# Optimization experiments

Measured on AMD Instinct MI355X. Metric: run time of the kernel, lower is better.

## Reference

```python
import jax, jax.numpy as jnp
import numpy as np

WIN = 11
K1 = 0.01
K2 = 0.03


def setup_inputs() -> dict:
    key = jax.random.key(0)
    k1, k2 = jax.random.split(key)
    B, C, H, W = 64, 1, 512, 512
    img = jax.random.uniform(k1, (B, C, H, W), dtype=jnp.float32)
    ref = jax.random.uniform(k2, (B, C, H, W), dtype=jnp.float32)
    data_range = jnp.ones((B,), dtype=jnp.float32)
    return {"img": img, "ref": ref, "data_range": data_range}


def _box_filter(x, win):
    w = jnp.ones((1, 1, win, win), dtype=x.dtype) / (win * win)
    pad = win // 2
    return jax.lax.conv_general_dilated(
        x, w, window_strides=(1, 1),
        padding=[(pad, pad), (pad, pad)],
        dimension_numbers=("NCHW", "OIHW", "NCHW"))


def reference(img, ref, data_range):
    dr = data_range[:, None, None, None]
    C1 = (K1 * dr) ** 2
    C2 = (K2 * dr) ** 2
    n_pix = WIN * WIN
    cov_norm = n_pix / (n_pix - 1)

    ux = _box_filter(img, WIN)
    uy = _box_filter(ref, WIN)
    uxx = _box_filter(img * img, WIN)
    uyy = _box_filter(ref * ref, WIN)
    uxy = _box_filter(img * ref, WIN)

    vx = cov_norm * (uxx - ux * ux)
    vy = cov_norm * (uyy - uy * uy)
    vxy = cov_norm * (uxy - ux * uy)

    A1 = 2 * ux * uy + C1
    A2 = 2 * vxy + C2
    B1 = ux ** 2 + uy ** 2 + C1
    B2 = vx + vy + C2
    S = A1 * A2 / (B1 * B2)
    return S
```

## Files before the change

kernel.cpp:

```cpp
#include <hip/hip_runtime.h>


static constexpr int HI = 512, WI = 512;
static constexpr int RS = 16;
static constexpr int SPB = HI / RS;

struct R8 { float4 a, b; };

__device__ __forceinline__ R8 ld8(const float* p) {
  R8 r; r.a = ((const float4*)p)[0]; r.b = ((const float4*)p)[1]; return r;
}

__device__ __forceinline__ void unp(const R8& v, float o[8]) {
  o[0]=v.a.x; o[1]=v.a.y; o[2]=v.a.z; o[3]=v.a.w;
  o[4]=v.b.x; o[5]=v.b.y; o[6]=v.b.z; o[7]=v.b.w;
}

__device__ __forceinline__ float shr1(float x) {
  return __int_as_float(__builtin_amdgcn_update_dpp(
      0, __float_as_int(x), 0x138, 0xf, 0xf, true));
}
__device__ __forceinline__ float shl1(float x) {
  return __int_as_float(__builtin_amdgcn_update_dpp(
      0, __float_as_int(x), 0x130, 0xf, 0xf, true));
}

__device__ __forceinline__ void horiz11(const float v[8], float H[8]) {
  float L[5], R[5];
#pragma unroll
  for (int k = 0; k < 5; ++k) {
    L[k] = shr1(v[3 + k]);
    R[k] = shl1(v[k]);
  }
  float h = (((L[0] + L[1]) + (L[2] + L[3])) + ((L[4] + v[0]) + (v[1] + v[2])))
            + ((v[3] + v[4]) + v[5]);
  H[0] = h;
  h = h - L[0] + v[6]; H[1] = h;
  h = h - L[1] + v[7]; H[2] = h;
  h = h - L[2] + R[0]; H[3] = h;
  h = h - L[3] + R[1]; H[4] = h;
  h = h - L[4] + R[2]; H[5] = h;
  h = h - v[0] + R[3]; H[6] = h;
  h = h - v[1] + R[4]; H[7] = h;
}

__global__ __launch_bounds__(256, 2)
void ssim_wave(const float* __restrict__ img, const float* __restrict__ ref,
               const float* __restrict__ drng, const float* __restrict__ zrow,
               float* __restrict__ out)
{
  int bid = (int)blockIdx.x;
  const int nb = (int)gridDim.x;
  if ((nb & 7) == 0) {
    const int cpx = nb >> 3;
    bid = (bid & 7) * cpx + (bid >> 3);
  }

  const int lane = threadIdx.x & 63;
  const int wv   = bid * 4 + (threadIdx.x >> 6);
  const int b    = wv / SPB;
  const int r0   = (wv % SPB) * RS;
  const int c0   = lane * 8;

  const float dr  = drng[b];
  const float C1  = (0.01f * dr) * (0.01f * dr);
  const float C2  = (0.03f * dr) * (0.03f * dr);
  const float inv_n    = 1.0f / 121.0f;
  const float cov_norm = 121.0f / 120.0f;

  const size_t base = (size_t)b * ((size_t)HI * WI);
  const float* xb = img + base;
  const float* yb = ref + base;
  float*       ob = out + base;

  auto nrow = [&](const float* tb, int t) -> const float* {
    const int r = r0 - 5 + t;
    return (((unsigned)r < (unsigned)HI) ? tb + (size_t)r * WI : zrow) + c0;
  };
  auto orow = [&](const float* tb, int t) -> const float* {
    const int r = r0 - 16 + t;
    return (((unsigned)r < (unsigned)HI) ? tb + (size_t)r * WI : zrow) + c0;
  };

  float Sx[8], Sy[8], Sxx[8], Syy[8], Sxy[8];
#pragma unroll
  for (int c = 0; c < 8; ++c) { Sx[c]=0.f; Sy[c]=0.f; Sxx[c]=0.f; Syy[c]=0.f; Sxy[c]=0.f; }

  auto accA = [&](const float xn[8], const float yn[8]) {
#pragma unroll
    for (int c = 0; c < 8; ++c) {
      Sx[c] += xn[c];  Sy[c] += yn[c];
      Sxx[c] = fmaf(xn[c], xn[c], Sxx[c]);
      Syy[c] = fmaf(yn[c], yn[c], Syy[c]);
      Sxy[c] = fmaf(xn[c], yn[c], Sxy[c]);
    }
  };
  auto accB = [&](const float xn[8], const float yn[8],
                  const float xo[8], const float yo[8]) {
#pragma unroll
    for (int c = 0; c < 8; ++c) {
      Sx[c] += xn[c] - xo[c];
      Sy[c] += yn[c] - yo[c];
      Sxx[c] = fmaf(xn[c], xn[c], fmaf(-xo[c], xo[c], Sxx[c]));
      Syy[c] = fmaf(yn[c], yn[c], fmaf(-yo[c], yo[c], Syy[c]));
      Sxy[c] = fmaf(xn[c], yn[c], fmaf(-xo[c], yo[c], Sxy[c]));
    }
  };

  auto emit = [&](int t) {
    float H0[8], H1[8], H2[8], H3[8], H4[8];
    horiz11(Sx,  H0);
    horiz11(Sy,  H1);
    horiz11(Sxx, H2);
    horiz11(Syy, H3);
    horiz11(Sxy, H4);
    float res[8];
#pragma unroll
    for (int c = 0; c < 8; ++c) {
      const float ux  = H0[c] * inv_n, uy  = H1[c] * inv_n;
      const float uxx = H2[c] * inv_n, uyy = H3[c] * inv_n, uxy = H4[c] * inv_n;
      const float vx  = cov_norm * (uxx - ux * ux);
      const float vy  = cov_norm * (uyy - uy * uy);
      const float vxy = cov_norm * (uxy - ux * uy);
      const float A1 = 2.f * ux * uy + C1;
      const float A2 = 2.f * vxy + C2;
      const float B1 = ux * ux + uy * uy + C1;
      const float B2 = vx + vy + C2;
      res[c] = (A1 * A2) * __builtin_amdgcn_rcpf(B1 * B2);
    }
    const int ro = r0 + t - 10;
    float4* po = (float4*)(ob + (size_t)ro * WI + c0);
    po[0] = make_float4(res[0], res[1], res[2], res[3]);
    po[1] = make_float4(res[4], res[5], res[6], res[7]);
  };

  R8 nx[2], ny[2], ox[2], oy[2];
  nx[0] = ld8(nrow(xb, 0)); ny[0] = ld8(nrow(yb, 0));
  nx[1] = ld8(nrow(xb, 1)); ny[1] = ld8(nrow(yb, 1));

#pragma unroll 2
  for (int t = 0; t < 9; ++t) {
    const int s = t & 1;
    float xn[8], yn[8];
    unp(nx[s], xn); unp(ny[s], yn);
    nx[s] = ld8(nrow(xb, t + 2)); ny[s] = ld8(nrow(yb, t + 2));
    accA(xn, yn);
  }
  {
    float xn[8], yn[8];
    unp(nx[1], xn); unp(ny[1], yn);
    nx[1] = ld8(nrow(xb, 11)); ny[1] = ld8(nrow(yb, 11));
    ox[1] = ld8(orow(xb, 11)); oy[1] = ld8(orow(yb, 11));
    accA(xn, yn);
  }
  {
    float xn[8], yn[8];
    unp(nx[0], xn); unp(ny[0], yn);
    nx[0] = ld8(nrow(xb, 12)); ny[0] = ld8(nrow(yb, 12));
    ox[0] = ld8(orow(xb, 12)); oy[0] = ld8(orow(yb, 12));
    accA(xn, yn);
    emit(10);
  }

  auto stepB = [&](int t, int s, bool issue) {
    float xn[8], yn[8], xo[8], yo[8];
    unp(nx[s], xn); unp(ny[s], yn); unp(ox[s], xo); unp(oy[s], yo);
    if (issue) {
      nx[s] = ld8(nrow(xb, t + 2)); ny[s] = ld8(nrow(yb, t + 2));
      ox[s] = ld8(orow(xb, t + 2)); oy[s] = ld8(orow(yb, t + 2));
    }
    accB(xn, yn, xo, yo);
    emit(t);
  };

#pragma unroll 1
  for (int u = 0; u < 6; ++u) {
    stepB(11 + 2 * u, 1, true);
    stepB(12 + 2 * u, 0, true);
  }
  stepB(23, 1, true);
  stepB(24, 0, false);
  stepB(25, 1, false);
}

extern "C" void kernel_launch(void* const* d_in, const int* in_sizes, int n_in,
                              void* d_out, int out_size, void* d_ws, size_t ws_size,
                              hipStream_t stream)
{
  const float* img = (const float*)d_in[0];
  const float* ref = (const float*)d_in[1];
  const float* drg = (const float*)d_in[2];
  float* out = (float*)d_out;

  (void)hipMemsetAsync(d_ws, 0, (size_t)WI * sizeof(float) + 64, stream);

  const int B = in_sizes[0] / (HI * WI);
  const int waves = B * SPB;
  dim3 grid(waves / 4);
  dim3 block(256);
  hipLaunchKernelGGL(ssim_wave, grid, block, 0, stream,
                     img, ref, drg, (const float*)d_ws, out);
}
```

Baseline: 208.1 us.

## Cache sliding-window rows in an LDS ring instead of reloading from global

Each wave now keeps the last 11 input rows of img and ref in a per-wave LDS ring buffer. The rows leaving the vertical window are read from that ring rather than reloaded from global memory, which removes the second global load stream. In exchange, each block needs about 90 KB of dynamic LDS and the block shrinks to 128 threads, so only about one block (two waves) fits per CU. That sharply cuts occupancy and the ability to hide latency.

```diff
diff --git a/kernel.cpp b/kernel.cpp
--- a/kernel.cpp
+++ b/kernel.cpp
@@ -4,6 +4,7 @@
 static constexpr int HI = 512, WI = 512;
 static constexpr int RS = 16;
 static constexpr int SPB = HI / RS;
+static constexpr int RINGB = 11 * 2 * (WI * 4);
 
 struct R8 { float4 a, b; };
 
@@ -44,11 +45,13 @@
   h = h - v[1] + R[4]; H[7] = h;
 }
 
-__global__ __launch_bounds__(256, 2)
+__global__ __launch_bounds__(128)
 void ssim_wave(const float* __restrict__ img, const float* __restrict__ ref,
                const float* __restrict__ drng, const float* __restrict__ zrow,
                float* __restrict__ out)
 {
+  extern __shared__ char lds_raw[];
+
   int bid = (int)blockIdx.x;
   const int nb = (int)gridDim.x;
   if ((nb & 7) == 0) {
@@ -56,11 +59,24 @@
     bid = (bid & 7) * cpx + (bid >> 3);
   }
 
-  const int lane = threadIdx.x & 63;
-  const int wv   = bid * 4 + (threadIdx.x >> 6);
-  const int b    = wv / SPB;
-  const int r0   = (wv % SPB) * RS;
-  const int c0   = lane * 8;
+  const int lane  = threadIdx.x & 63;
+  const int wslot = threadIdx.x >> 6;
+  const int wv    = bid * 2 + wslot;
+  const int b     = wv / SPB;
+  const int r0    = (wv % SPB) * RS;
+  const int c0    = lane * 8;
+
+  float4* ring = (float4*)(lds_raw + wslot * RINGB);
+  auto ringw = [&](int slot, const R8& vx, const R8& vy) {
+    float4* p = ring + slot * 256 + lane * 2;
+    p[0] = vx.a; p[1] = vx.b;
+    p[128] = vy.a; p[129] = vy.b;
+  };
+  auto ringr = [&](int slot, R8& vx, R8& vy) {
+    float4* p = ring + slot * 256 + lane * 2;
+    vx.a = p[0]; vx.b = p[1];
+    vy.a = p[128]; vy.b = p[129];
+  };
 
   const float dr  = drng[b];
   const float C1  = (0.01f * dr) * (0.01f * dr);
@@ -75,10 +91,6 @@
 
   auto nrow = [&](const float* tb, int t) -> const float* {
     const int r = r0 - 5 + t;
-    return (((unsigned)r < (unsigned)HI) ? tb + (size_t)r * WI : zrow) + c0;
-  };
-  auto orow = [&](const float* tb, int t) -> const float* {
-    const int r = r0 - 16 + t;
     return (((unsigned)r < (unsigned)HI) ? tb + (size_t)r * WI : zrow) + c0;
   };
 
@@ -134,41 +146,29 @@
     po[1] = make_float4(res[4], res[5], res[6], res[7]);
   };
 
-  R8 nx[2], ny[2], ox[2], oy[2];
+  R8 nx[2], ny[2];
   nx[0] = ld8(nrow(xb, 0)); ny[0] = ld8(nrow(yb, 0));
   nx[1] = ld8(nrow(xb, 1)); ny[1] = ld8(nrow(yb, 1));
 
 #pragma unroll 2
-  for (int t = 0; t < 9; ++t) {
+  for (int t = 0; t < 11; ++t) {
     const int s = t & 1;
     float xn[8], yn[8];
     unp(nx[s], xn); unp(ny[s], yn);
-    nx[s] = ld8(nrow(xb, t + 2)); ny[s] = ld8(nrow(yb, t + 2));
+    ringw(t, nx[s], ny[s]);
+    if (t + 2 < 26) { nx[s] = ld8(nrow(xb, t + 2)); ny[s] = ld8(nrow(yb, t + 2)); }
     accA(xn, yn);
-  }
-  {
-    float xn[8], yn[8];
-    unp(nx[1], xn); unp(ny[1], yn);
-    nx[1] = ld8(nrow(xb, 11)); ny[1] = ld8(nrow(yb, 11));
-    ox[1] = ld8(orow(xb, 11)); oy[1] = ld8(orow(yb, 11));
-    accA(xn, yn);
-  }
-  {
-    float xn[8], yn[8];
-    unp(nx[0], xn); unp(ny[0], yn);
-    nx[0] = ld8(nrow(xb, 12)); ny[0] = ld8(nrow(yb, 12));
-    ox[0] = ld8(orow(xb, 12)); oy[0] = ld8(orow(yb, 12));
-    accA(xn, yn);
-    emit(10);
+    if (t == 10) emit(10);
   }
 
   auto stepB = [&](int t, int s, bool issue) {
+    const int slot = (t >= 22) ? (t - 22) : (t - 11);
+    R8 oxr, oyr;
+    ringr(slot, oxr, oyr);
+    ringw(slot, nx[s], ny[s]);
     float xn[8], yn[8], xo[8], yo[8];
-    unp(nx[s], xn); unp(ny[s], yn); unp(ox[s], xo); unp(oy[s], yo);
-    if (issue) {
-      nx[s] = ld8(nrow(xb, t + 2)); ny[s] = ld8(nrow(yb, t + 2));
-      ox[s] = ld8(orow(xb, t + 2)); oy[s] = ld8(orow(yb, t + 2));
-    }
+    unp(nx[s], xn); unp(ny[s], yn); unp(oxr, xo); unp(oyr, yo);
+    if (issue) { nx[s] = ld8(nrow(xb, t + 2)); ny[s] = ld8(nrow(yb, t + 2)); }
     accB(xn, yn, xo, yo);
     emit(t);
   };
@@ -192,12 +192,20 @@
   const float* drg = (const float*)d_in[2];
   float* out = (float*)d_out;
 
+  static bool attr_done = false;
+  if (!attr_done) {
+    (void)hipFuncSetAttribute((const void*)ssim_wave,
+                              hipFuncAttributeMaxDynamicSharedMemorySize,
+                              2 * RINGB);
+    attr_done = true;
+  }
+
   (void)hipMemsetAsync(d_ws, 0, (size_t)WI * sizeof(float) + 64, stream);
 
   const int B = in_sizes[0] / (HI * WI);
   const int waves = B * SPB;
-  dim3 grid(waves / 4);
-  dim3 block(256);
-  hipLaunchKernelGGL(ssim_wave, grid, block, 0, stream,
+  dim3 grid(waves / 2);
+  dim3 block(128);
+  hipLaunchKernelGGL(ssim_wave, grid, block, 2 * RINGB, stream,
                      img, ref, drg, (const float*)d_ws, out);
 }
```

After: 227.3 us. 1.09x slower.
